# Performance work log

Hardware: AMD Instinct MI355X
Metric: run time of the kernel (lower is better)

Reference implementation:

```python
import jax, jax.numpy as jnp
import numpy as np

NEG_SLOPE = 0.1

def lrelu(x):
    return jnp.where(x > 0, x, NEG_SLOPE * x)

def conv3(x, w, b):
    # 3x3 conv, stride 1, pad 1, NCHW / OIHW
    y = jax.lax.conv_general_dilated(x, w, (1, 1), ((1, 1), (1, 1)),
                                     dimension_numbers=('NCHW', 'OIHW', 'NCHW'))
    return y + b[None, :, None, None]

def correlation(f1, f2, stride):
    # 7x7 windowed cost volume, displacements in {-3..3}*stride, zero pad, /C
    B, C, H, W = f1.shape
    pad = 3 * stride
    f1s = f1[:, :, ::stride, ::stride]                      # [B,C,Ho,Wo] (ceil)
    f2p = jnp.pad(f2, ((0, 0), (0, 0), (pad, pad), (pad, pad)))
    outs = []
    for dy in range(7):
        for dx in range(7):
            sl = f2p[:, :, dy * stride: dy * stride + H: stride,
                           dx * stride: dx * stride + W: stride]
            outs.append(jnp.sum(f1s * sl, axis=1))           # [B,Ho,Wo]
    return jnp.stack(outs, axis=1) / C                       # [B,49,Ho,Wo]

def apply_offset(offset):
    # offset: [B,2,H,W]; channel 0 = x displacement, 1 = y displacement
    B, _, H, W = offset.shape
    gx = jnp.arange(W, dtype=offset.dtype)[None, None, :] + offset[:, 0]
    gy = jnp.arange(H, dtype=offset.dtype)[None, :, None] + offset[:, 1]
    gx = gx / ((W - 1.0) / 2.0) - 1.0
    gy = gy / ((H - 1.0) / 2.0) - 1.0
    return jnp.stack([gx, gy], axis=-1)                      # [B,H,W,2]

def grid_sample(img, grid):
    # bilinear, padding_mode='border', align_corners=True
    B, C, H, W = img.shape
    x = jnp.clip((grid[..., 0] + 1.0) * 0.5 * (W - 1), 0.0, W - 1.0)
    y = jnp.clip((grid[..., 1] + 1.0) * 0.5 * (H - 1), 0.0, H - 1.0)
    x0 = jnp.floor(x); y0 = jnp.floor(y)
    wx = x - x0; wy = y - y0
    x0 = x0.astype(jnp.int32); y0 = y0.astype(jnp.int32)
    x1 = jnp.minimum(x0 + 1, W - 1); y1 = jnp.minimum(y0 + 1, H - 1)
    imgf = img.reshape(B, C, H * W)
    def gather(yy, xx):
        idx = (yy * W + xx).reshape(B, 1, H * W)
        g = jnp.take_along_axis(imgf, jnp.broadcast_to(idx, (B, C, H * W)), axis=2)
        return g.reshape(B, C, H, W)
    wx = wx[:, None]; wy = wy[:, None]
    return (gather(y0, x0) * (1 - wx) * (1 - wy) + gather(y0, x1) * wx * (1 - wy)
            + gather(y1, x0) * (1 - wx) * wy + gather(y1, x1) * wx * wy)

def setup_inputs() -> dict:
    key = jax.random.key(0)
    ks = jax.random.split(key, 12)
    B, C, H, W = 8, 256, 128, 96
    s = 0.05
    return {
        'feat1': jax.random.normal(ks[0], (B, C, H, W), jnp.float32),
        'feat2': jax.random.normal(ks[1], (B, C, H, W), jnp.float32),
        'w1': s * jax.random.normal(ks[2], (128, 49, 3, 3), jnp.float32),
        'b1': jnp.zeros((128,), jnp.float32),
        'w2': s * jax.random.normal(ks[3], (64, 128, 3, 3), jnp.float32),
        'b2': jnp.zeros((64,), jnp.float32),
        'w3': s * jax.random.normal(ks[4], (32, 64, 3, 3), jnp.float32),
        'b3': jnp.zeros((32,), jnp.float32),
        'w4': s * jax.random.normal(ks[5], (2, 32, 3, 3), jnp.float32),
        'b4': jnp.zeros((2,), jnp.float32),
        'stride': 1,
    }

def reference(feat1, feat2, w1, b1, w2, b2, w3, b3, w4, b4, stride):
    corr = lrelu(correlation(feat1, feat2, stride))          # [B,49,H,W]
    h = lrelu(conv3(corr, w1, b1))
    h = lrelu(conv3(h, w2, b2))
    h = lrelu(conv3(h, w3, b3))
    flow = conv3(h, w4, b4)                                  # [B,2,H,W]
    grid = apply_offset(flow)
    warped = grid_sample(feat2, grid)                        # [B,C,H,W]
    return warped
```

## Files before the change

### kernel.cpp

```cpp
#include <hip/hip_runtime.h>

constexpr int B_ = 8, C_ = 256, H_ = 128, W_ = 96;
constexpr int HW_ = H_ * W_;

typedef __bf16 bf16x8 __attribute__((ext_vector_type(8)));
typedef float f32x4 __attribute__((ext_vector_type(4)));

__device__ __forceinline__ float lrelu_f(float v) { return v > 0.f ? v : 0.1f * v; }
__device__ __forceinline__ ushort f2b(float v) {
    __bf16 h = (__bf16)v;
    return __builtin_bit_cast(ushort, h);
}
__device__ __forceinline__ float blo(unsigned u) {
    return __builtin_bit_cast(float, u << 16);
}
__device__ __forceinline__ float bhi(unsigned u) {
    return __builtin_bit_cast(float, u & 0xffff0000u);
}

constexpr int CR = 4;
constexpr int F2R = 12;
constexpr int CCH = 8;

__global__ __launch_bounds__(768)
void corr_kernel(const float* __restrict__ f1, const float* __restrict__ f2,
                 ushort* __restrict__ corr_nhwc)
{
    __shared__ __align__(16) float s2[F2R][CCH][128];
    __shared__ __align__(16) float s1[CCH][CR][96];

    const int tid = threadIdx.x;
    const int pxg = tid % 24;
    const int ty = (tid / 24) % CR;
    const int dy = tid / 96;
    const int x0 = pxg * 4;

    const int b = blockIdx.x >> 5;
    const int y0 = (blockIdx.x & 31) * CR;

    float acc[7][4];
#pragma unroll
    for (int j = 0; j < 7; j++)
#pragma unroll
        for (int k = 0; k < 4; k++) acc[j][k] = 0.f;

    const float* f1p = f1 + b * C_ * HW_;
    const float* f2p = f2 + b * C_ * HW_;

    for (int cc = 0; cc < C_; cc += CCH) {
        __syncthreads();
#pragma unroll
        for (int k = 0; k < 16; k++) {
            int e = k * 768 + tid;
            int col = e & 127;
            int c = (e >> 7) & 7;
            int r = e >> 10;
            int yg = y0 + r - 3;
            int xg = col - 3;
            bool valid = ((unsigned)yg < (unsigned)H_) && ((unsigned)xg < (unsigned)W_);
            int ygc = min(max(yg, 0), H_ - 1);
            int xgc = min(max(xg, 0), W_ - 1);
            float v = f2p[(cc + c) * HW_ + ygc * W_ + xgc];
            s2[r][c][col] = valid ? v : 0.f;
        }
#pragma unroll
        for (int k = 0; k < 4; k++) {
            int e = k * 768 + tid;
            int idx = e / 96;
            int col = e - idx * 96;
            int c = idx >> 2;
            int r = idx & 3;
            s1[c][r][col] = f1p[(cc + c) * HW_ + (y0 + r) * W_ + col];
        }
        __syncthreads();
#pragma unroll
        for (int c = 0; c < CCH; c++) {
            float4 v1 = *(const float4*)&s1[c][ty][x0];
            float v1a[4] = {v1.x, v1.y, v1.z, v1.w};
            const float* rp = &s2[ty + dy][c][x0];
            float4 a0 = *(const float4*)&rp[0];
            float4 a1 = *(const float4*)&rp[4];
            float4 a2 = *(const float4*)&rp[8];
            float iv[12] = {a0.x, a0.y, a0.z, a0.w, a1.x, a1.y, a1.z, a1.w,
                            a2.x, a2.y, a2.z, a2.w};
#pragma unroll
            for (int dx = 0; dx < 7; dx++)
#pragma unroll
                for (int p = 0; p < 4; p++)
                    acc[dx][p] += v1a[p] * iv[p + dx];
        }
    }

    __syncthreads();
    ushort* t = (ushort*)&s2[0][0][0];
    const float scale = 1.f / 256.f;
    if (dy < 7) {
#pragma unroll
        for (int dx = 0; dx < 7; dx++)
#pragma unroll
            for (int p = 0; p < 4; p++)
                t[(ty * 96 + x0 + p) * 64 + dy * 7 + dx] =
                    f2b(lrelu_f(acc[dx][p] * scale));
    } else {
#pragma unroll
        for (int p = 0; p < 4; p++)
            for (int c = 49; c < 64; c++)
                t[(ty * 96 + x0 + p) * 64 + c] = 0;
    }
    __syncthreads();
    const uint4* src = (const uint4*)t;
    uint4* dst = (uint4*)(corr_nhwc + (size_t)(b * HW_ + y0 * W_) * 64);
    for (int e = tid; e < 3072; e += 768) dst[e] = src[e];
}

template <int CIN, int COUT, int CIP>
__global__ __launch_bounds__(256)
void pack_w(const float* __restrict__ w, ushort* __restrict__ wpk)
{
    int i = blockIdx.x * 256 + threadIdx.x;
    if (i >= 9 * COUT * CIP) return;
    int ci = i % CIP;
    int t = i / CIP;
    int oc = t % COUT;
    int tap = t / COUT;
    float v = (ci < CIN) ? w[(oc * CIN + ci) * 9 + tap] : 0.f;
    wpk[i] = f2b(v);
}

template <int CIP, int COUT, int OCB, int XT, int XTILES>
__global__ __launch_bounds__(256)
void conv_mfma(const ushort* __restrict__ in, const ushort* __restrict__ wpk,
               const float* __restrict__ bias, ushort* __restrict__ out)
{
    constexpr int OCF = OCB / 16, PXF = XT / 16, COLS = XT + 2;
    constexpr int G = CIP / 8, KC = CIP / 32;
    __shared__ __align__(16) ushort sIn[6 * COLS * CIP];

    const int tid = threadIdx.x;
    const int lane = tid & 63;
    const int ty = tid >> 6;
    const int ln = lane & 15;
    const int lq = lane >> 4;

    const int gx = blockIdx.x;
    const int xt = gx % XTILES;
    const int yt = (gx / XTILES) % 32;
    const int b = gx / (XTILES * 32);
    const int oc0 = blockIdx.y * OCB;
    const int x0 = xt * XT;
    const int y0 = yt * 4;

    constexpr int NU = 6 * COLS * G;
    for (int e = tid; e < NU; e += 256) {
        int g = e & (G - 1);
        int pc = e / G;
        int col = pc % COLS;
        int rr = pc / COLS;
        int yg = y0 - 1 + rr;
        int xg = x0 - 1 + col;
        uint4 v = make_uint4(0, 0, 0, 0);
        if ((unsigned)yg < (unsigned)H_ && (unsigned)xg < (unsigned)W_)
            v = *(const uint4*)(in + ((size_t)(b * HW_ + yg * W_ + xg) * CIP + g * 8));
        int p = rr * COLS + col;
        *(uint4*)(sIn + (size_t)(p * G + (g ^ (p & 7))) * 8) = v;
    }
    __syncthreads();

    f32x4 acc[OCF][PXF];
#pragma unroll
    for (int of = 0; of < OCF; of++)
#pragma unroll
        for (int pf = 0; pf < PXF; pf++) {
            f32x4 z = {0.f, 0.f, 0.f, 0.f};
            acc[of][pf] = z;
        }

    const uint4* wq = (const uint4*)wpk;
    for (int kc = 0; kc < KC; kc++) {
        for (int tap = 0; tap < 9; tap++) {
            const int r = tap / 3, s = tap % 3;
            bf16x8 afr[OCF];
#pragma unroll
            for (int of = 0; of < OCF; of++) {
                int off = ((tap * COUT + oc0 + of * 16 + ln) * CIP + kc * 32 + lq * 8) >> 3;
                afr[of] = __builtin_bit_cast(bf16x8, wq[off]);
            }
#pragma unroll
            for (int pf = 0; pf < PXF; pf++) {
                int p = (ty + r) * COLS + (pf * 16 + ln + s);
                int g = kc * 4 + lq;
                uint4 bv = *(const uint4*)(sIn + (size_t)(p * G + (g ^ (p & 7))) * 8);
                bf16x8 bfr = __builtin_bit_cast(bf16x8, bv);
#pragma unroll
                for (int of = 0; of < OCF; of++)
                    acc[of][pf] = __builtin_amdgcn_mfma_f32_16x16x32_bf16(
                        afr[of], bfr, acc[of][pf], 0, 0, 0);
            }
        }
    }

    const int y = y0 + ty;
#pragma unroll
    for (int of = 0; of < OCF; of++) {
        int ocb = oc0 + of * 16 + lq * 4;
        float4 bv = *(const float4*)(bias + ocb);
        float bs[4] = {bv.x, bv.y, bv.z, bv.w};
#pragma unroll
        for (int pf = 0; pf < PXF; pf++) {
            int x = x0 + pf * 16 + ln;
            ushort4 pk;
            pk.x = f2b(lrelu_f(acc[of][pf][0] + bs[0]));
            pk.y = f2b(lrelu_f(acc[of][pf][1] + bs[1]));
            pk.z = f2b(lrelu_f(acc[of][pf][2] + bs[2]));
            pk.w = f2b(lrelu_f(acc[of][pf][3] + bs[3]));
            *(ushort4*)(out + ((size_t)(b * HW_ + y * W_ + x) * COUT + ocb)) = pk;
        }
    }
}

__global__ __launch_bounds__(256)
void conv4_kernel(const ushort* __restrict__ in, const float* __restrict__ wgt,
                  const float* __restrict__ bias, float* __restrict__ flow)
{
    __shared__ float s_w[2 * 9 * 32];
    const int tid = threadIdx.x;
    for (int e = tid; e < 576; e += 256) {
        int ci = e & 31;
        int t = e >> 5;
        int tap = t % 9;
        int oc = t / 9;
        s_w[e] = wgt[(oc * 32 + ci) * 9 + tap];
    }
    __syncthreads();

    int pix = blockIdx.x * 256 + tid;
    int b = pix / HW_;
    int rem = pix - b * HW_;
    int yy = rem / W_;
    int xx = rem - yy * W_;

    float a0 = bias[0], a1 = bias[1];
    for (int tap = 0; tap < 9; tap++) {
        int r = tap / 3, s = tap % 3;
        int yg = yy + r - 1, xg = xx + s - 1;
        if ((unsigned)yg >= (unsigned)H_ || (unsigned)xg >= (unsigned)W_) continue;
        const uint4* p = (const uint4*)(in + (size_t)(b * HW_ + yg * W_ + xg) * 32);
        const float* w0 = &s_w[(0 * 9 + tap) * 32];
        const float* w1 = &s_w[(1 * 9 + tap) * 32];
#pragma unroll
        for (int q = 0; q < 4; q++) {
            uint4 v = p[q];
            unsigned uu[4] = {v.x, v.y, v.z, v.w};
#pragma unroll
            for (int h = 0; h < 4; h++) {
                int ci = q * 8 + h * 2;
                float vl = blo(uu[h]), vh = bhi(uu[h]);
                a0 += vl * w0[ci] + vh * w0[ci + 1];
                a1 += vl * w1[ci] + vh * w1[ci + 1];
            }
        }
    }
    flow[(b * 2 + 0) * HW_ + rem] = a0;
    flow[(b * 2 + 1) * HW_ + rem] = a1;
}

__global__ __launch_bounds__(256)
void warp_kernel(const float* __restrict__ f2, const float* __restrict__ flow,
                 float* __restrict__ out)
{
    int pix = blockIdx.x * 256 + threadIdx.x;
    int cbase = blockIdx.y * 64;
    int b = pix / HW_;
    int rem = pix - b * HW_;
    int yy = rem / W_;
    int xx = rem - yy * W_;

    float fx = flow[(b * 2 + 0) * HW_ + rem];
    float fy = flow[(b * 2 + 1) * HW_ + rem];
    float xs = fminf(fmaxf((float)xx + fx, 0.f), (float)(W_ - 1));
    float ys = fminf(fmaxf((float)yy + fy, 0.f), (float)(H_ - 1));
    float x0f = floorf(xs), y0f = floorf(ys);
    int x0 = (int)x0f, y0 = (int)y0f;
    float wx = xs - x0f, wy = ys - y0f;
    int x1 = min(x0 + 1, W_ - 1), y1 = min(y0 + 1, H_ - 1);

    int i00 = y0 * W_ + x0, i01 = y0 * W_ + x1;
    int i10 = y1 * W_ + x0, i11 = y1 * W_ + x1;
    float w00 = (1.f - wx) * (1.f - wy), w01 = wx * (1.f - wy);
    float w10 = (1.f - wx) * wy, w11 = wx * wy;

    const float* base = f2 + (size_t)(b * C_ + cbase) * HW_;
    float* ob = out + (size_t)(b * C_ + cbase) * HW_ + rem;
#pragma unroll 4
    for (int c = 0; c < 64; c++) {
        const float* p = base + c * HW_;
        ob[c * HW_] = p[i00] * w00 + p[i01] * w01 + p[i10] * w10 + p[i11] * w11;
    }
}

extern "C" void kernel_launch(void* const* d_in, const int* in_sizes, int n_in,
                              void* d_out, int out_size, void* d_ws, size_t ws_size,
                              hipStream_t stream)
{
    (void)in_sizes; (void)n_in; (void)out_size; (void)ws_size;
    const float* feat1 = (const float*)d_in[0];
    const float* feat2 = (const float*)d_in[1];
    const float* w1 = (const float*)d_in[2];
    const float* b1 = (const float*)d_in[3];
    const float* w2 = (const float*)d_in[4];
    const float* b2 = (const float*)d_in[5];
    const float* w3 = (const float*)d_in[6];
    const float* b3 = (const float*)d_in[7];
    const float* w4 = (const float*)d_in[8];
    const float* b4 = (const float*)d_in[9];

    char* ws = (char*)d_ws;
    ushort* corr_nhwc = (ushort*)(ws);
    ushort* h1 = (ushort*)(ws + 12582912);
    ushort* h2 = (ushort*)(ws + 37748736);
    ushort* h3 = (ushort*)(ws + 50331648);
    float* flow = (float*)(ws + 56623104);
    ushort* wpk1 = (ushort*)(ws + 57409536);
    ushort* wpk2 = (ushort*)(ws + 57556992);
    ushort* wpk3 = (ushort*)(ws + 57704448);
    float* out = (float*)d_out;

    pack_w<49, 128, 64><<<288, 256, 0, stream>>>(w1, wpk1);
    pack_w<128, 64, 128><<<288, 256, 0, stream>>>(w2, wpk2);
    pack_w<64, 32, 64><<<72, 256, 0, stream>>>(w3, wpk3);

    corr_kernel<<<256, 768, 0, stream>>>(feat1, feat2, corr_nhwc);
    conv_mfma<64, 128, 64, 48, 2><<<dim3(512, 2), 256, 0, stream>>>(corr_nhwc, wpk1, b1, h1);
    conv_mfma<128, 64, 64, 32, 3><<<dim3(768, 1), 256, 0, stream>>>(h1, wpk2, b2, h2);
    conv_mfma<64, 32, 32, 48, 2><<<dim3(512, 1), 256, 0, stream>>>(h2, wpk3, b3, h3);
    conv4_kernel<<<384, 256, 0, stream>>>(h3, w4, b4, flow);
    warp_kernel<<<dim3(384, 4), 256, 0, stream>>>(feat2, flow, out);
}
```

Measured before the change: 514.0 us.

## Double-buffer correlation staging with direct global-to-LDS loads and XOR swizzle

Replaces the register-staged global loads in the correlation kernel with global_load_lds direct-to-LDS transfers into two ping-pong buffers, so the next channel chunk loads while the current one is computed. Column indices are XOR-swizzled to reduce LDS bank conflicts. Out-of-bounds padding now reads from a zeroed scratch region that is memset in the workspace. This doubles LDS use, which may limit occupancy. It also relies on the scratch region (h3) being zero when the correlation kernel runs, before h3 is overwritten later.

Result: slower. 723.6 us (+40.8%).

```diff
diff --git a/kernel.cpp b/kernel.cpp
--- a/kernel.cpp
+++ b/kernel.cpp
@@ -18,16 +18,25 @@
     return __builtin_bit_cast(float, u & 0xffff0000u);
 }
 
+typedef __attribute__((address_space(1))) void gas_void;
+typedef __attribute__((address_space(3))) void las_void;
+__device__ __forceinline__ void gl_lds4(const float* g, float* l) {
+    __builtin_amdgcn_global_load_lds((gas_void*)g, (las_void*)l, 4, 0, 0);
+}
+
 constexpr int CR = 4;
 constexpr int F2R = 12;
 constexpr int CCH = 8;
 
 __global__ __launch_bounds__(768)
 void corr_kernel(const float* __restrict__ f1, const float* __restrict__ f2,
+                 const float* __restrict__ zero_src,
                  ushort* __restrict__ corr_nhwc)
 {
-    __shared__ __align__(16) float s2[F2R][CCH][128];
-    __shared__ __align__(16) float s1[CCH][CR][96];
+    __shared__ __align__(16) float s2a[F2R * CCH * 128];
+    __shared__ __align__(16) float s2b[F2R * CCH * 128];
+    __shared__ __align__(16) float s1a[CCH * CR * 96];
+    __shared__ __align__(16) float s1b[CCH * CR * 96];
 
     const int tid = threadIdx.x;
     const int pxg = tid % 24;
@@ -47,40 +56,47 @@
     const float* f1p = f1 + b * C_ * HW_;
     const float* f2p = f2 + b * C_ * HW_;
 
-    for (int cc = 0; cc < C_; cc += CCH) {
-        __syncthreads();
+    auto STAGE = [&](int cc, float* s2d, float* s1d) {
 #pragma unroll
         for (int k = 0; k < 16; k++) {
             int e = k * 768 + tid;
-            int col = e & 127;
+            int colp = e & 127;
             int c = (e >> 7) & 7;
             int r = e >> 10;
+            int coll = colp ^ ((r & 7) << 2);
             int yg = y0 + r - 3;
-            int xg = col - 3;
+            int xg = coll - 3;
             bool valid = ((unsigned)yg < (unsigned)H_) && ((unsigned)xg < (unsigned)W_);
             int ygc = min(max(yg, 0), H_ - 1);
             int xgc = min(max(xg, 0), W_ - 1);
-            float v = f2p[(cc + c) * HW_ + ygc * W_ + xgc];
-            s2[r][c][col] = valid ? v : 0.f;
+            const float* src = valid ? (f2p + (cc + c) * HW_ + ygc * W_ + xgc)
+                                     : zero_src;
+            gl_lds4(src, s2d + e);
         }
 #pragma unroll
         for (int k = 0; k < 4; k++) {
             int e = k * 768 + tid;
             int idx = e / 96;
-            int col = e - idx * 96;
+            int colp = e - idx * 96;
             int c = idx >> 2;
             int r = idx & 3;
-            s1[c][r][col] = f1p[(cc + c) * HW_ + (y0 + r) * W_ + col];
-        }
-        __syncthreads();
+            int coll = colp ^ ((r & 3) << 2);
+            gl_lds4(f1p + (cc + c) * HW_ + (y0 + r) * W_ + coll, s1d + e);
+        }
+    };
+
+    auto COMPUTE = [&](const float* s2c, const float* s1c) {
+        const int r = ty + dy;
+        const int sw2 = (r & 7) << 2;
+        const int sw1 = (ty & 3) << 2;
 #pragma unroll
         for (int c = 0; c < CCH; c++) {
-            float4 v1 = *(const float4*)&s1[c][ty][x0];
+            float4 v1 = *(const float4*)&s1c[(c * CR + ty) * 96 + (x0 ^ sw1)];
             float v1a[4] = {v1.x, v1.y, v1.z, v1.w};
-            const float* rp = &s2[ty + dy][c][x0];
-            float4 a0 = *(const float4*)&rp[0];
-            float4 a1 = *(const float4*)&rp[4];
-            float4 a2 = *(const float4*)&rp[8];
+            const float* rp = &s2c[(r * CCH + c) * 128];
+            float4 a0 = *(const float4*)&rp[x0 ^ sw2];
+            float4 a1 = *(const float4*)&rp[(x0 + 4) ^ sw2];
+            float4 a2 = *(const float4*)&rp[(x0 + 8) ^ sw2];
             float iv[12] = {a0.x, a0.y, a0.z, a0.w, a1.x, a1.y, a1.z, a1.w,
                             a2.x, a2.y, a2.z, a2.w};
 #pragma unroll
@@ -89,10 +105,22 @@
                 for (int p = 0; p < 4; p++)
                     acc[dx][p] += v1a[p] * iv[p + dx];
         }
-    }
-
+    };
+
+    STAGE(0, s2a, s1a);
     __syncthreads();
-    ushort* t = (ushort*)&s2[0][0][0];
+
+#pragma unroll 1
+    for (int cc = 0; cc < C_; cc += 2 * CCH) {
+        STAGE(cc + CCH, s2b, s1b);
+        COMPUTE(s2a, s1a);
+        __syncthreads();
+        if (cc + 2 * CCH < C_) STAGE(cc + 2 * CCH, s2a, s1a);
+        COMPUTE(s2b, s1b);
+        __syncthreads();
+    }
+
+    ushort* t = (ushort*)s2a;
     const float scale = 1.f / 256.f;
     if (dy < 7) {
 #pragma unroll
@@ -325,11 +353,14 @@
     ushort* wpk3 = (ushort*)(ws + 57704448);
     float* out = (float*)d_out;
 
+    float* zero_src = (float*)(ws + 50331648);
+    hipMemsetAsync(zero_src, 0, 256, stream);
+
     pack_w<49, 128, 64><<<288, 256, 0, stream>>>(w1, wpk1);
     pack_w<128, 64, 128><<<288, 256, 0, stream>>>(w2, wpk2);
     pack_w<64, 32, 64><<<72, 256, 0, stream>>>(w3, wpk3);
 
-    corr_kernel<<<256, 768, 0, stream>>>(feat1, feat2, corr_nhwc);
+    corr_kernel<<<256, 768, 0, stream>>>(feat1, feat2, zero_src, corr_nhwc);
     conv_mfma<64, 128, 64, 48, 2><<<dim3(512, 2), 256, 0, stream>>>(corr_nhwc, wpk1, b1, h1);
     conv_mfma<128, 64, 64, 32, 3><<<dim3(768, 1), 256, 0, stream>>>(h1, wpk2, b2, h2);
     conv_mfma<64, 32, 32, 48, 2><<<dim3(512, 1), 256, 0, stream>>>(h2, wpk3, b3, h3);
```

## Split correlation channel reduction across two blocks and swizzle shared memory

Applied to the files above, without the earlier changes.

The correlation kernel's 256-channel reduction is split into two halves handled by separate blocks, which doubles the grid from 256 to 512 blocks to improve CU occupancy. Each half writes fp32 partial sums to workspace, and a new reduce kernel adds them, applies scale, leaky ReLU and bf16 conversion, then writes NHWC output. Shared-memory indices are XOR-swizzled to cut bank conflicts on the float4 loads. The cost is an extra launch and a round trip of partial sums through global memory, with the partials buffer reusing the h1 workspace region.

Measured after the change: 502.1 us. 2.3% less time.

```diff
diff --git a/kernel.cpp b/kernel.cpp
--- a/kernel.cpp
+++ b/kernel.cpp
@@ -23,11 +23,11 @@
 constexpr int CCH = 8;
 
 __global__ __launch_bounds__(768)
-void corr_kernel(const float* __restrict__ f1, const float* __restrict__ f2,
-                 ushort* __restrict__ corr_nhwc)
-{
-    __shared__ __align__(16) float s2[F2R][CCH][128];
-    __shared__ __align__(16) float s1[CCH][CR][96];
+void corr_split(const float* __restrict__ f1, const float* __restrict__ f2,
+                float* __restrict__ P)
+{
+    __shared__ __align__(16) float s2[F2R * CCH * 128];
+    __shared__ __align__(16) float s1[CCH * CR * 96];
 
     const int tid = threadIdx.x;
     const int pxg = tid % 24;
@@ -35,8 +35,11 @@
     const int dy = tid / 96;
     const int x0 = pxg * 4;
 
-    const int b = blockIdx.x >> 5;
-    const int y0 = (blockIdx.x & 31) * CR;
+    const int bid = blockIdx.x;
+    const int h = bid & 1;
+    const int t = bid >> 1;
+    const int b = t >> 5;
+    const int y0 = (t & 31) * CR;
 
     float acc[7][4];
 #pragma unroll
@@ -47,7 +50,12 @@
     const float* f1p = f1 + b * C_ * HW_;
     const float* f2p = f2 + b * C_ * HW_;
 
-    for (int cc = 0; cc < C_; cc += CCH) {
+    const int sw2 = ((ty + dy) & 7) << 2;
+    const int xa = x0 ^ sw2, xb = (x0 + 4) ^ sw2, xc = (x0 + 8) ^ sw2;
+    const int xd = x0 ^ (ty << 2);
+
+    const int c0 = h * 128;
+    for (int cc = c0; cc < c0 + 128; cc += CCH) {
         __syncthreads();
 #pragma unroll
         for (int k = 0; k < 16; k++) {
@@ -61,7 +69,7 @@
             int ygc = min(max(yg, 0), H_ - 1);
             int xgc = min(max(xg, 0), W_ - 1);
             float v = f2p[(cc + c) * HW_ + ygc * W_ + xgc];
-            s2[r][c][col] = valid ? v : 0.f;
+            s2[(r * CCH + c) * 128 + (col ^ ((r & 7) << 2))] = valid ? v : 0.f;
         }
 #pragma unroll
         for (int k = 0; k < 4; k++) {
@@ -70,17 +78,18 @@
             int col = e - idx * 96;
             int c = idx >> 2;
             int r = idx & 3;
-            s1[c][r][col] = f1p[(cc + c) * HW_ + (y0 + r) * W_ + col];
+            s1[(c * CR + r) * 96 + (col ^ (r << 2))] =
+                f1p[(cc + c) * HW_ + (y0 + r) * W_ + col];
         }
         __syncthreads();
 #pragma unroll
         for (int c = 0; c < CCH; c++) {
-            float4 v1 = *(const float4*)&s1[c][ty][x0];
+            float4 v1 = *(const float4*)&s1[(c * CR + ty) * 96 + xd];
             float v1a[4] = {v1.x, v1.y, v1.z, v1.w};
-            const float* rp = &s2[ty + dy][c][x0];
-            float4 a0 = *(const float4*)&rp[0];
-            float4 a1 = *(const float4*)&rp[4];
-            float4 a2 = *(const float4*)&rp[8];
+            const float* rp = &s2[((ty + dy) * CCH + c) * 128];
+            float4 a0 = *(const float4*)&rp[xa];
+            float4 a1 = *(const float4*)&rp[xb];
+            float4 a2 = *(const float4*)&rp[xc];
             float iv[12] = {a0.x, a0.y, a0.z, a0.w, a1.x, a1.y, a1.z, a1.w,
                             a2.x, a2.y, a2.z, a2.w};
 #pragma unroll
@@ -91,16 +100,44 @@
         }
     }
 
-    __syncthreads();
-    ushort* t = (ushort*)&s2[0][0][0];
+    if (dy < 7) {
+        float* pb = P + ((size_t)(h * 256 + t) * 49 + dy * 7) * 384 + ty * 96 + x0;
+#pragma unroll
+        for (int dx = 0; dx < 7; dx++) {
+            float4 v = {acc[dx][0], acc[dx][1], acc[dx][2], acc[dx][3]};
+            *(float4*)(pb + dx * 384) = v;
+        }
+    }
+}
+
+__global__ __launch_bounds__(768)
+void corr_reduce(const float* __restrict__ P, ushort* __restrict__ corr_nhwc)
+{
+    __shared__ __align__(16) ushort t[4 * 96 * 64];
+
+    const int tid = threadIdx.x;
+    const int pxg = tid % 24;
+    const int ty = (tid / 24) % CR;
+    const int dy = tid / 96;
+    const int x0 = pxg * 4;
+    const int ti = blockIdx.x;
+    const int b = ti >> 5;
+    const int y0 = (ti & 31) * CR;
+
     const float scale = 1.f / 256.f;
     if (dy < 7) {
-#pragma unroll
-        for (int dx = 0; dx < 7; dx++)
+        const float* p0 = P + ((size_t)(0 * 256 + ti) * 49 + dy * 7) * 384 + ty * 96 + x0;
+        const float* p1 = P + ((size_t)(1 * 256 + ti) * 49 + dy * 7) * 384 + ty * 96 + x0;
+#pragma unroll
+        for (int dx = 0; dx < 7; dx++) {
+            float4 a = *(const float4*)(p0 + dx * 384);
+            float4 c = *(const float4*)(p1 + dx * 384);
+            float s[4] = {a.x + c.x, a.y + c.y, a.z + c.z, a.w + c.w};
 #pragma unroll
             for (int p = 0; p < 4; p++)
                 t[(ty * 96 + x0 + p) * 64 + dy * 7 + dx] =
-                    f2b(lrelu_f(acc[dx][p] * scale));
+                    f2b(lrelu_f(s[p] * scale));
+        }
     } else {
 #pragma unroll
         for (int p = 0; p < 4; p++)
@@ -325,11 +362,14 @@
     ushort* wpk3 = (ushort*)(ws + 57704448);
     float* out = (float*)d_out;
 
+    float* Ppart = (float*)(ws + 12582912);
+
     pack_w<49, 128, 64><<<288, 256, 0, stream>>>(w1, wpk1);
     pack_w<128, 64, 128><<<288, 256, 0, stream>>>(w2, wpk2);
     pack_w<64, 32, 64><<<72, 256, 0, stream>>>(w3, wpk3);
 
-    corr_kernel<<<256, 768, 0, stream>>>(feat1, feat2, corr_nhwc);
+    corr_split<<<512, 768, 0, stream>>>(feat1, feat2, Ppart);
+    corr_reduce<<<256, 768, 0, stream>>>(Ppart, corr_nhwc);
     conv_mfma<64, 128, 64, 48, 2><<<dim3(512, 2), 256, 0, stream>>>(corr_nhwc, wpk1, b1, h1);
     conv_mfma<128, 64, 64, 32, 3><<<dim3(768, 1), 256, 0, stream>>>(h1, wpk2, b2, h2);
     conv_mfma<64, 32, 32, 48, 2><<<dim3(512, 1), 256, 0, stream>>>(h2, wpk3, b3, h3);
```
